# Kernel tuning notes

Measured on AMD Instinct MI355X. Metric: run time of the kernel, lower is better.

The kernel has to match this reference:

```python
import jax, jax.numpy as jnp
import numpy as np

UNITS = 256
IN_DIM = 256
OUT_DIM = 10
TOL = 1e-4
MAX_ITER = 50


def setup_inputs() -> dict:
    key = jax.random.key(0)
    ks = jax.random.split(key, 16)
    B = 65536
    s = 1.0 / np.sqrt(UNITS)
    inp = {
        "x": jax.random.normal(ks[0], (B, IN_DIM), dtype=jnp.float32),
        "w_in": jax.random.normal(ks[1], (IN_DIM, UNITS), dtype=jnp.float32) * s,
        "b_in": jax.random.normal(ks[2], (UNITS,), dtype=jnp.float32) * 0.01,
        "w_out": jax.random.normal(ks[3], (UNITS, OUT_DIM), dtype=jnp.float32) * s,
        "b_out": jax.random.normal(ks[4], (OUT_DIM,), dtype=jnp.float32) * 0.01,
    }
    eye = jnp.eye(UNITS, dtype=jnp.float32)
    for i in range(4):
        # well-conditioned (invertible) implicit-layer weight: I + small perturbation
        inp[f"w{i+1}"] = eye + 0.1 * jax.random.normal(ks[5 + 2 * i], (UNITS, UNITS), dtype=jnp.float32) * s
        inp[f"b{i+1}"] = jax.random.normal(ks[6 + 2 * i], (UNITS,), dtype=jnp.float32) * 0.01
    return inp


def newton_block(x, W, b):
    # Solve z @ W = x + tanh(x) + b by Newton iteration with early exit on ||g||.
    c = x + jnp.tanh(x) + b  # [B, n]
    z0 = x
    g0 = z0 @ W - c

    def cond(state):
        z, g, it = state
        return (it < MAX_ITER) & (jnp.linalg.norm(g) >= TOL)

    def body(state):
        z, g, it = state
        # torch.solve(g[:, :, None], W^T.repeat(B,1,1)): shared matrix -> one solve
        z = z - jnp.linalg.solve(W.T, g.T).T
        g = z @ W - c
        return (z, g, it + 1)

    z, _, _ = jax.lax.while_loop(cond, body, (z0, g0, jnp.asarray(0)))
    z = jax.lax.stop_gradient(z)  # torch loop runs under no_grad
    # final differentiable correction (torch: z = z - (z@W - x - tanh(x) - b))
    return z - (z @ W - c)


def reference(x, w_in, b_in, w1, b1, w2, b2, w3, b3, w4, b4, w_out, b_out):
    z = x @ w_in + b_in
    z = newton_block(z, w1, b1)
    z = newton_block(z, w2, b2)
    z = newton_block(z, w3, b3)
    z = newton_block(z, w4, b4)
    logits = z @ w_out + b_out
    return jax.nn.softmax(logits, axis=1)
```

## Files before the change

### kernel.cpp

```cpp
#include <hip/hip_runtime.h>
#include <hip/hip_fp16.h>
#include <math.h>


typedef __attribute__((ext_vector_type(8))) short short8;
typedef __attribute__((ext_vector_type(4))) float f32x4;

__device__ __forceinline__ float tanh_fast(float x) {
#if __has_builtin(__builtin_amdgcn_exp2f)
  float e = __builtin_amdgcn_exp2f(x * 2.8853900817779268f);
#else
  float e = __expf(2.0f * x);
#endif
  return 1.0f - 2.0f * __builtin_amdgcn_rcpf(e + 1.0f);
}
__device__ __forceinline__ unsigned rn_pair16(float v0, float v1) {
  __half2 h = __floats2half2_rn(v0, v1);
  return *reinterpret_cast<unsigned*>(&h);
}
__device__ __forceinline__ unsigned rtz_pair16(float v0, float v1) {
#if __has_builtin(__builtin_amdgcn_cvt_pkrtz)
  typedef __fp16 h2v __attribute__((ext_vector_type(2)));
  h2v h = __builtin_amdgcn_cvt_pkrtz(v0, v1);
  return *reinterpret_cast<unsigned*>(&h);
#else
  return rn_pair16(v0, v1);
#endif
}

__global__ __launch_bounds__(256) void ns_poly_k(
    const float* __restrict__ w1, const float* __restrict__ w2,
    const float* __restrict__ w3, const float* __restrict__ w4,
    const float* __restrict__ w_in, const float* __restrict__ w_out,
    unsigned* __restrict__ pk) {
  const int bid = blockIdx.x;
  const int t = threadIdx.x;
  if (bid >= 256) {
    int idx = (bid - 256) * 256 + t;
    {
      int kc = idx >> 12;
      int nt = (idx >> 8) & 15;
      int lane = (idx >> 2) & 63;
      int d = idx & 3;
      int n = nt * 16 + (lane & 15);
      int kb = kc * 32 + (lane >> 4) * 8 + d * 2;
      pk[idx] = rn_pair16(w_in[kb * 256 + n], w_in[(kb + 1) * 256 + n]);
    }
    int idx2 = idx + 32768;
    if (idx2 < 34816) {
      int r2 = idx2 - 32768;
      int kc = r2 >> 8;
      int lane = (r2 >> 2) & 63;
      int d = r2 & 3;
      int n = lane & 15;
      int kb = kc * 32 + (lane >> 4) * 8 + d * 2;
      float v0 = (n < 10) ? w_out[kb * 10 + n] : 0.0f;
      float v1 = (n < 10) ? w_out[(kb + 1) * 10 + n] : 0.0f;
      pk[5 * 32768 + r2] = rn_pair16(v0, v1);
    }
    return;
  }
  const int m = bid >> 6;
  const int r0 = (bid & 63) * 4;
  const float* __restrict__ W = (m == 0) ? w1 : (m == 1) ? w2 : (m == 2) ? w3 : w4;
  __shared__ float S[4][256];

#pragma unroll
  for (int i = 0; i < 4; ++i) {
    int e = i * 256 + t;
    int r = e >> 8, c = e & 255;
    S[r][c] = (((r0 + r) == c) ? 6.0f : 0.0f) - W[(r0 + r) * 256 + c];
  }
  __syncthreads();

  const float coef[4] = {-15.0f, 20.0f, -15.0f, 6.0f};
#pragma unroll
  for (int step = 0; step < 4; ++step) {
    float acc[4];
#pragma unroll
    for (int r = 0; r < 4; ++r) acc[r] = 0.0f;
    for (int k = 0; k < 256; k += 4) {
      float4 sv[4];
#pragma unroll
      for (int r = 0; r < 4; ++r) sv[r] = *(const float4*)&S[r][k];
      float wv0 = W[(k + 0) * 256 + t];
      float wv1 = W[(k + 1) * 256 + t];
      float wv2 = W[(k + 2) * 256 + t];
      float wv3 = W[(k + 3) * 256 + t];
#pragma unroll
      for (int r = 0; r < 4; ++r) {
        acc[r] = fmaf(sv[r].x, wv0, acc[r]);
        acc[r] = fmaf(sv[r].y, wv1, acc[r]);
        acc[r] = fmaf(sv[r].z, wv2, acc[r]);
        acc[r] = fmaf(sv[r].w, wv3, acc[r]);
      }
    }
    __syncthreads();
    float cdiag = coef[step];
#pragma unroll
    for (int r = 0; r < 4; ++r)
      S[r][t] = acc[r] + (((r0 + r) == t) ? cdiag : 0.0f);
    __syncthreads();
  }

  const int kc = r0 >> 5;
  const int quad = (r0 >> 3) & 3;
  const int d0 = (r0 & 7) >> 1;
#pragma unroll
  for (int i = 0; i < 2; ++i) {
    int q = i * 256 + t;
    int nt = q >> 5;
    int n16 = (q >> 1) & 15;
    int dd = q & 1;
    int n = nt * 16 + n16;
    int lane = quad * 16 + n16;
    unsigned word = rn_pair16(S[2 * dd][n], S[2 * dd + 1][n]);
    pk[(m + 1) * 32768 + kc * 4096 + nt * 256 + lane * 4 + (d0 + dd)] = word;
  }
}

template <int MT>
__global__ __launch_bounds__(256, 4) void fused_k(
    const float* __restrict__ x, const unsigned* __restrict__ pk,
    const float* __restrict__ b_in,
    const float* __restrict__ b1, const float* __restrict__ b2,
    const float* __restrict__ b3, const float* __restrict__ b4,
    const float* __restrict__ b_out, float* __restrict__ out) {
  constexpr int NR = MT * 16;
  __shared__ unsigned short zpl[NR * 256];
  const int t = threadIdx.x;
  const int ln = t & 63;
  const int wv = t >> 6;
  const int quad = ln >> 4;
  const int n16 = ln & 15;
  const int grow0 = blockIdx.x * NR;

#pragma unroll
  for (int i = 0; i < MT * 4; ++i) {
    int e = i * 1024 + t * 4;
    int r = e >> 8, c = e & 255;
    float4 v = *(const float4*)(x + (grow0 + r) * 256 + c);
    int idx = r * 256 + (((c >> 3) ^ (r & 31)) * 8) + (c & 7);
    uint2 zp;
    zp.x = rtz_pair16(v.x, v.y);
    zp.y = rtz_pair16(v.z, v.w);
    *(uint2*)&zpl[idx] = zp;
  }
  __syncthreads();

  const float* bnv[4] = {b1, b2, b3, b4};
  f32x4 acc[MT][4];

  for (int layer = 0; layer < 5; ++layer) {
    const unsigned* pkl = pk + layer * 32768 + wv * 1024 + ln * 4;
#pragma unroll
    for (int mt = 0; mt < MT; ++mt)
#pragma unroll
      for (int nt = 0; nt < 4; ++nt) acc[mt][nt] = (f32x4){0.f, 0.f, 0.f, 0.f};

#pragma unroll 2
    for (int kc = 0; kc < 8; ++kc) {
      short8 wh[4], zf[MT];
      const unsigned* pb = pkl + kc * 4096;
#pragma unroll
      for (int nt = 0; nt < 4; ++nt) wh[nt] = *(const short8*)(pb + nt * 256);
#pragma unroll
      for (int mt = 0; mt < MT; ++mt) {
        int mm = mt * 16 + n16;
        int idx = mm * 256 + (((kc * 4 + quad) ^ (mm & 31)) * 8);
        zf[mt] = *(const short8*)&zpl[idx];
      }
#pragma unroll
      for (int mt = 0; mt < MT; ++mt)
#pragma unroll
        for (int nt = 0; nt < 4; ++nt)
          acc[mt][nt] = __builtin_amdgcn_mfma_f32_16x16x32_f16(wh[nt], zf[mt], acc[mt][nt], 0, 0, 0);
    }
    __syncthreads();

#pragma unroll
    for (int nt = 0; nt < 4; ++nt) {
      int colb = wv * 64 + nt * 16 + quad * 4;
      float4 bi = make_float4(0.f, 0.f, 0.f, 0.f);
      float4 bn4 = bi;
      if (layer == 0) bi = *(const float4*)(b_in + colb);
      if (layer < 4) bn4 = *(const float4*)(bnv[layer] + colb);
#pragma unroll
      for (int mt = 0; mt < MT; ++mt) {
        int row = mt * 16 + n16;
        float v0 = acc[mt][nt][0] + bi.x;
        float v1 = acc[mt][nt][1] + bi.y;
        float v2 = acc[mt][nt][2] + bi.z;
        float v3 = acc[mt][nt][3] + bi.w;
        if (layer < 4) {
          v0 = v0 + tanh_fast(v0) + bn4.x;
          v1 = v1 + tanh_fast(v1) + bn4.y;
          v2 = v2 + tanh_fast(v2) + bn4.z;
          v3 = v3 + tanh_fast(v3) + bn4.w;
        }
        int idx = row * 256 + (((colb >> 3) ^ (row & 31)) * 8) + (colb & 7);
        uint2 zp;
        zp.x = rtz_pair16(v0, v1);
        zp.y = rtz_pair16(v2, v3);
        *(uint2*)&zpl[idx] = zp;
      }
    }
    __syncthreads();
  }

  f32x4 lacc[MT];
#pragma unroll
  for (int mt = 0; mt < MT; ++mt) lacc[mt] = (f32x4){0.f, 0.f, 0.f, 0.f};
  const unsigned* pw = pk + 5 * 32768 + ln * 4;
#pragma unroll
  for (int kk = 0; kk < 2; ++kk) {
    int kc = wv * 2 + kk;
    short8 wh = *(const short8*)(pw + kc * 256);
#pragma unroll
    for (int mt = 0; mt < MT; ++mt) {
      int mm = mt * 16 + n16;
      int idx = mm * 256 + (((kc * 4 + quad) ^ (mm & 31)) * 8);
      short8 zf = *(const short8*)&zpl[idx];
      lacc[mt] = __builtin_amdgcn_mfma_f32_16x16x32_f16(wh, zf, lacc[mt], 0, 0, 0);
    }
  }
  __syncthreads();
  float* pbuf = (float*)zpl;
#pragma unroll
  for (int mt = 0; mt < MT; ++mt) {
    int addr = wv * (NR * 16) + (mt * 16 + n16) * 16 + quad * 4;
    *(f32x4*)&pbuf[addr] = lacc[mt];
  }
  __syncthreads();
  if (t < NR) {
    int r = t;
    float lg[10];
    float mx = -1e30f;
#pragma unroll
    for (int j = 0; j < 10; ++j) {
      float s = b_out[j];
#pragma unroll
      for (int w2 = 0; w2 < 4; ++w2) s += pbuf[w2 * (NR * 16) + r * 16 + j];
      lg[j] = s;
      mx = fmaxf(mx, s);
    }
    float sum = 0.f;
#pragma unroll
    for (int j = 0; j < 10; ++j) {
      lg[j] = __expf(lg[j] - mx);
      sum += lg[j];
    }
    float inv = 1.0f / sum;
    float* op = out + (grow0 + r) * 10;
#pragma unroll
    for (int j = 0; j < 10; ++j) op[j] = lg[j] * inv;
  }
}

extern "C" void kernel_launch(void* const* d_in, const int* in_sizes, int n_in,
                              void* d_out, int out_size, void* d_ws, size_t ws_size,
                              hipStream_t stream) {
  const float* x     = (const float*)d_in[0];
  const float* w_in  = (const float*)d_in[1];
  const float* b_in  = (const float*)d_in[2];
  const float* w_out = (const float*)d_in[3];
  const float* b_out = (const float*)d_in[4];
  const float* w1 = (const float*)d_in[5];
  const float* b1 = (const float*)d_in[6];
  const float* w2 = (const float*)d_in[7];
  const float* b2 = (const float*)d_in[8];
  const float* w3 = (const float*)d_in[9];
  const float* b3 = (const float*)d_in[10];
  const float* w4 = (const float*)d_in[11];
  const float* b4 = (const float*)d_in[12];
  float* out = (float*)d_out;

  unsigned* pk = (unsigned*)d_ws;

  ns_poly_k<<<384, 256, 0, stream>>>(w1, w2, w3, w4, w_in, w_out, pk);
  fused_k<4><<<1024, 256, 0, stream>>>(x, pk, b_in, b1, b2, b3, b4, b_out, out);
}
```

Baseline: 183.1 us.

## Merge weight-prep and fused kernels into one launch with a global semaphore

Folds the Newton-Schulz polynomial weight packing into the first 384 blocks of the main fused kernel. Those blocks signal completion through an atomic counter, and every block spins on that counter after staging its x tile. The aim is to remove the gap between the two launches and overlap the x load with weight preparation. The cost is an extra memset, a spin-wait with deadlock risk if not all producer blocks are resident, and the prep work now runs at the occupancy of the main kernel.

```diff
diff --git a/kernel.cpp b/kernel.cpp
--- a/kernel.cpp
+++ b/kernel.cpp
@@ -28,112 +28,115 @@
 #endif
 }
 
-__global__ __launch_bounds__(256) void ns_poly_k(
+#define NPROD 384
+
+__global__ __launch_bounds__(256, 4) void mono_k(
+    const float* __restrict__ x, unsigned* __restrict__ pk,
+    unsigned* __restrict__ sem,
+    const float* __restrict__ w_in, const float* __restrict__ w_out,
     const float* __restrict__ w1, const float* __restrict__ w2,
     const float* __restrict__ w3, const float* __restrict__ w4,
-    const float* __restrict__ w_in, const float* __restrict__ w_out,
-    unsigned* __restrict__ pk) {
-  const int bid = blockIdx.x;
-  const int t = threadIdx.x;
-  if (bid >= 256) {
-    int idx = (bid - 256) * 256 + t;
-    {
-      int kc = idx >> 12;
-      int nt = (idx >> 8) & 15;
-      int lane = (idx >> 2) & 63;
-      int d = idx & 3;
-      int n = nt * 16 + (lane & 15);
-      int kb = kc * 32 + (lane >> 4) * 8 + d * 2;
-      pk[idx] = rn_pair16(w_in[kb * 256 + n], w_in[(kb + 1) * 256 + n]);
-    }
-    int idx2 = idx + 32768;
-    if (idx2 < 34816) {
-      int r2 = idx2 - 32768;
-      int kc = r2 >> 8;
-      int lane = (r2 >> 2) & 63;
-      int d = r2 & 3;
-      int n = lane & 15;
-      int kb = kc * 32 + (lane >> 4) * 8 + d * 2;
-      float v0 = (n < 10) ? w_out[kb * 10 + n] : 0.0f;
-      float v1 = (n < 10) ? w_out[(kb + 1) * 10 + n] : 0.0f;
-      pk[5 * 32768 + r2] = rn_pair16(v0, v1);
-    }
-    return;
-  }
-  const int m = bid >> 6;
-  const int r0 = (bid & 63) * 4;
-  const float* __restrict__ W = (m == 0) ? w1 : (m == 1) ? w2 : (m == 2) ? w3 : w4;
-  __shared__ float S[4][256];
-
-#pragma unroll
-  for (int i = 0; i < 4; ++i) {
-    int e = i * 256 + t;
-    int r = e >> 8, c = e & 255;
-    S[r][c] = (((r0 + r) == c) ? 6.0f : 0.0f) - W[(r0 + r) * 256 + c];
-  }
-  __syncthreads();
-
-  const float coef[4] = {-15.0f, 20.0f, -15.0f, 6.0f};
-#pragma unroll
-  for (int step = 0; step < 4; ++step) {
-    float acc[4];
-#pragma unroll
-    for (int r = 0; r < 4; ++r) acc[r] = 0.0f;
-    for (int k = 0; k < 256; k += 4) {
-      float4 sv[4];
-#pragma unroll
-      for (int r = 0; r < 4; ++r) sv[r] = *(const float4*)&S[r][k];
-      float wv0 = W[(k + 0) * 256 + t];
-      float wv1 = W[(k + 1) * 256 + t];
-      float wv2 = W[(k + 2) * 256 + t];
-      float wv3 = W[(k + 3) * 256 + t];
-#pragma unroll
-      for (int r = 0; r < 4; ++r) {
-        acc[r] = fmaf(sv[r].x, wv0, acc[r]);
-        acc[r] = fmaf(sv[r].y, wv1, acc[r]);
-        acc[r] = fmaf(sv[r].z, wv2, acc[r]);
-        acc[r] = fmaf(sv[r].w, wv3, acc[r]);
-      }
-    }
-    __syncthreads();
-    float cdiag = coef[step];
-#pragma unroll
-    for (int r = 0; r < 4; ++r)
-      S[r][t] = acc[r] + (((r0 + r) == t) ? cdiag : 0.0f);
-    __syncthreads();
-  }
-
-  const int kc = r0 >> 5;
-  const int quad = (r0 >> 3) & 3;
-  const int d0 = (r0 & 7) >> 1;
-#pragma unroll
-  for (int i = 0; i < 2; ++i) {
-    int q = i * 256 + t;
-    int nt = q >> 5;
-    int n16 = (q >> 1) & 15;
-    int dd = q & 1;
-    int n = nt * 16 + n16;
-    int lane = quad * 16 + n16;
-    unsigned word = rn_pair16(S[2 * dd][n], S[2 * dd + 1][n]);
-    pk[(m + 1) * 32768 + kc * 4096 + nt * 256 + lane * 4 + (d0 + dd)] = word;
-  }
-}
-
-template <int MT>
-__global__ __launch_bounds__(256, 4) void fused_k(
-    const float* __restrict__ x, const unsigned* __restrict__ pk,
     const float* __restrict__ b_in,
     const float* __restrict__ b1, const float* __restrict__ b2,
     const float* __restrict__ b3, const float* __restrict__ b4,
     const float* __restrict__ b_out, float* __restrict__ out) {
+  constexpr int MT = 4;
   constexpr int NR = MT * 16;
   __shared__ unsigned short zpl[NR * 256];
   const int t = threadIdx.x;
+  const int bid = blockIdx.x;
   const int ln = t & 63;
   const int wv = t >> 6;
   const int quad = ln >> 4;
   const int n16 = ln & 15;
-  const int grow0 = blockIdx.x * NR;
+  const int grow0 = bid * NR;
+
+  if (bid < NPROD) {
+    if (bid >= 256) {
+      int idx = (bid - 256) * 256 + t;
+      {
+        int kc = idx >> 12;
+        int nt = (idx >> 8) & 15;
+        int lane = (idx >> 2) & 63;
+        int d = idx & 3;
+        int n = nt * 16 + (lane & 15);
+        int kb = kc * 32 + (lane >> 4) * 8 + d * 2;
+        pk[idx] = rn_pair16(w_in[kb * 256 + n], w_in[(kb + 1) * 256 + n]);
+      }
+      int idx2 = idx + 32768;
+      if (idx2 < 34816) {
+        int r2 = idx2 - 32768;
+        int kc = r2 >> 8;
+        int lane = (r2 >> 2) & 63;
+        int d = r2 & 3;
+        int n = lane & 15;
+        int kb = kc * 32 + (lane >> 4) * 8 + d * 2;
+        float v0 = (n < 10) ? w_out[kb * 10 + n] : 0.0f;
+        float v1 = (n < 10) ? w_out[(kb + 1) * 10 + n] : 0.0f;
+        pk[5 * 32768 + r2] = rn_pair16(v0, v1);
+      }
+    } else {
+      const int m = bid >> 6;
+      const int r0 = (bid & 63) * 4;
+      const float* __restrict__ W = (m == 0) ? w1 : (m == 1) ? w2 : (m == 2) ? w3 : w4;
+      float* S = (float*)zpl;
+#pragma unroll
+      for (int i = 0; i < 4; ++i) {
+        int e = i * 256 + t;
+        int r = e >> 8, c = e & 255;
+        S[r * 256 + c] = (((r0 + r) == c) ? 6.0f : 0.0f) - W[(r0 + r) * 256 + c];
+      }
+      __syncthreads();
+      const float coef[4] = {-15.0f, 20.0f, -15.0f, 6.0f};
+#pragma unroll
+      for (int step = 0; step < 4; ++step) {
+        float acc[4];
+#pragma unroll
+        for (int r = 0; r < 4; ++r) acc[r] = 0.0f;
+        for (int k = 0; k < 256; k += 4) {
+          float4 sv[4];
+#pragma unroll
+          for (int r = 0; r < 4; ++r) sv[r] = *(const float4*)&S[r * 256 + k];
+          float wv0 = W[(k + 0) * 256 + t];
+          float wv1 = W[(k + 1) * 256 + t];
+          float wv2 = W[(k + 2) * 256 + t];
+          float wv3 = W[(k + 3) * 256 + t];
+#pragma unroll
+          for (int r = 0; r < 4; ++r) {
+            acc[r] = fmaf(sv[r].x, wv0, acc[r]);
+            acc[r] = fmaf(sv[r].y, wv1, acc[r]);
+            acc[r] = fmaf(sv[r].z, wv2, acc[r]);
+            acc[r] = fmaf(sv[r].w, wv3, acc[r]);
+          }
+        }
+        __syncthreads();
+        float cdiag = coef[step];
+#pragma unroll
+        for (int r = 0; r < 4; ++r)
+          S[r * 256 + t] = acc[r] + (((r0 + r) == t) ? cdiag : 0.0f);
+        __syncthreads();
+      }
+      const int kc = r0 >> 5;
+      const int q4 = (r0 >> 3) & 3;
+      const int d0 = (r0 & 7) >> 1;
+#pragma unroll
+      for (int i = 0; i < 2; ++i) {
+        int q = i * 256 + t;
+        int nt = q >> 5;
+        int nn = (q >> 1) & 15;
+        int dd = q & 1;
+        unsigned word = rn_pair16(S[(2 * dd) * 256 + nt * 16 + nn],
+                                  S[(2 * dd + 1) * 256 + nt * 16 + nn]);
+        pk[(m + 1) * 32768 + kc * 4096 + nt * 256 + (q4 * 16 + nn) * 4 + (d0 + dd)] = word;
+      }
+    }
+    __syncthreads();
+    if (t == 0) {
+      __threadfence();
+      atomicAdd(sem, 1u);
+    }
+    __syncthreads();
+  }
 
 #pragma unroll
   for (int i = 0; i < MT * 4; ++i) {
@@ -145,6 +148,12 @@
     zp.x = rtz_pair16(v.x, v.y);
     zp.y = rtz_pair16(v.z, v.w);
     *(uint2*)&zpl[idx] = zp;
+  }
+
+  if (t == 0) {
+    while (__hip_atomic_load(sem, __ATOMIC_RELAXED, __HIP_MEMORY_SCOPE_AGENT) < NPROD)
+      __builtin_amdgcn_s_sleep(2);
+    __threadfence();
   }
   __syncthreads();
 
@@ -276,7 +285,10 @@
   float* out = (float*)d_out;
 
   unsigned* pk = (unsigned*)d_ws;
-
-  ns_poly_k<<<384, 256, 0, stream>>>(w1, w2, w3, w4, w_in, w_out, pk);
-  fused_k<4><<<1024, 256, 0, stream>>>(x, pk, b_in, b1, b2, b3, b4, b_out, out);
-}
+  unsigned* sem = pk + 165888;
+
+  hipMemsetAsync(sem, 0, 4, stream);
+  mono_k<<<1024, 256, 0, stream>>>(x, pk, sem, w_in, w_out,
+                                   w1, w2, w3, w4,
+                                   b_in, b1, b2, b3, b4, b_out, out);
+}
```

Measured after the change: 232.7 us. 1.27x slower.
